# Performance work log

Hardware: AMD Instinct MI355X
Metric: run time of the kernel (lower is better)

The kernel has to match this reference:

```python
import jax, jax.numpy as jnp
import numpy as np

N_NODES = 100000
N_EDGES = 1600000
IN_CH, HID_CH, OUT_CH = 64, 64, 16
N_REL = 8


def setup_inputs() -> dict:
    key = jax.random.key(0)
    ks = jax.random.split(key, 10)
    x = jax.random.normal(ks[0], (N_NODES, IN_CH), dtype=jnp.float32)
    edge_index = jax.random.randint(ks[1], (2, N_EDGES), 0, N_NODES, dtype=jnp.int64)
    edge_type = jax.random.randint(ks[2], (N_EDGES,), 0, N_REL, dtype=jnp.int64)
    # RGCNConv params: per-relation weight, root weight, bias (Glorot-ish scale)
    def glorot(k, shape):
        fan = shape[-2] + shape[-1]
        return jax.random.normal(k, shape, dtype=jnp.float32) * jnp.sqrt(2.0 / fan)
    W1 = glorot(ks[3], (N_REL, IN_CH, HID_CH))
    root1 = glorot(ks[4], (IN_CH, HID_CH))
    b1 = jnp.zeros((HID_CH,), dtype=jnp.float32)
    W2 = glorot(ks[5], (N_REL, HID_CH, OUT_CH))
    root2 = glorot(ks[6], (HID_CH, OUT_CH))
    b2 = jnp.zeros((OUT_CH,), dtype=jnp.float32)
    return {"x": x, "edge_index": edge_index, "edge_type": edge_type,
            "W1": W1, "root1": root1, "b1": b1,
            "W2": W2, "root2": root2, "b2": b2}


def rgcn_conv(x, src, dst, edge_type, W_rel, W_root, bias):
    """PyG RGCNConv: out_i = x_i @ W_root + b + sum_r mean_{j in N_r(i)} x_j @ W_r.
    Mean is linear, so aggregate raw features per relation, then transform."""
    n = x.shape[0]
    xs = x[src]  # [E, F] gathered source features (hot memory-bound op)
    out = x @ W_root + bias
    for r in range(W_rel.shape[0]):  # small fixed relation count
        mask = (edge_type == r).astype(x.dtype)  # [E]
        agg = jax.ops.segment_sum(xs * mask[:, None], dst, num_segments=n)  # [N, F]
        cnt = jax.ops.segment_sum(mask, dst, num_segments=n)  # [N]
        agg = agg / jnp.clip(cnt, 1.0)[:, None]  # mean aggr; 0 when no edges
        out = out + agg @ W_rel[r]
    return out


def reference(x, edge_index, edge_type, W1, root1, b1, W2, root2, b2):
    src, dst = edge_index[0], edge_index[1]
    h = rgcn_conv(x, src, dst, edge_type, W1, root1, b1)
    h = jax.nn.relu(h)
    h = rgcn_conv(h, src, dst, edge_type, W2, root2, b2)
    # global_mean_pool with a single graph: mean over nodes -> [1, out]
    g = jnp.mean(h, axis=0, keepdims=True)
    return jax.nn.log_softmax(g, axis=1)
```

## Files before the change

kernel.cpp:

```cpp
#include <hip/hip_runtime.h>
#include <hip/hip_bf16.h>


#define CH 64
#define BK_EDGES 2048
#define CAP 12288
#define RPT 12

typedef __attribute__((ext_vector_type(8))) short short8;
typedef __attribute__((ext_vector_type(4))) float f32x4;
typedef __attribute__((ext_vector_type(2))) float f32x2;

__device__ inline ushort f2bf(float f) {
    unsigned b = __float_as_uint(f);
    unsigned r = (b + 0x7FFFu + ((b >> 16) & 1u)) >> 16;
    return (ushort)r;
}
__device__ inline float bf2f(ushort u) {
    return __uint_as_float(((unsigned)u) << 16);
}

__device__ inline void acc8fp8(float* a, uint2 w, float m) {
    f32x2 p;
    p = __builtin_amdgcn_cvt_pk_f32_fp8(w.x, 0); a[0] += m * p.x; a[1] += m * p.y;
    p = __builtin_amdgcn_cvt_pk_f32_fp8(w.x, 1); a[2] += m * p.x; a[3] += m * p.y;
    p = __builtin_amdgcn_cvt_pk_f32_fp8(w.y, 0); a[4] += m * p.x; a[5] += m * p.y;
    p = __builtin_amdgcn_cvt_pk_f32_fp8(w.y, 1); a[6] += m * p.x; a[7] += m * p.y;
}


__global__ __launch_bounds__(256) void prep_kernel(
    const int* __restrict__ src, const int* __restrict__ dst,
    const int* __restrict__ etype, const float* __restrict__ x,
    const float* __restrict__ W1, const float* __restrict__ root1,
    int* __restrict__ gBucketCnt, int2* __restrict__ bucket_buf,
    ushort* __restrict__ xbf, unsigned char* __restrict__ xq,
    ushort* __restrict__ wf,
    int E, int N, int nBin, int nXbf)
{
    __shared__ int s_k[BK_EDGES];
    __shared__ int s_y[BK_EDGES];
    __shared__ int hist[256], scanv[256], lcur[256], bstart[256], gbase[256];
    const int t = threadIdx.x;
    const int bid = blockIdx.x;

    if (bid >= nBin) {
        if (bid < nBin + nXbf) {
            int i = (bid - nBin) * 256 + t;
            if (i < N * CH / 4) {
                float4 v = ((const float4*)x)[i];
                ((ushort4*)xbf)[i] = make_ushort4(f2bf(v.x), f2bf(v.y), f2bf(v.z), f2bf(v.w));
                int p8 = __builtin_amdgcn_cvt_pk_fp8_f32(v.x, v.y, 0, 0);
                p8 = __builtin_amdgcn_cvt_pk_fp8_f32(v.z, v.w, p8, 1);
                ((unsigned int*)xq)[i] = (unsigned int)p8;
            }
        } else {
            int idx = (bid - nBin - nXbf) * 256 + t;
            if (idx < 9 * 2 * 4 * 64 * 8) {
                int j    = idx & 7;
                int lane = (idx >> 3) & 63;
                int ct   = (idx >> 9) & 3;
                int ks   = (idx >> 11) & 1;
                int rel  = idx >> 12;
                int k = ks * 32 + (lane >> 4) * 8 + j;
                int n = ct * 16 + (lane & 15);
                float v = (rel < 8) ? W1[((size_t)rel * 64 + k) * 64 + n]
                                    : root1[(size_t)k * 64 + n];
                wf[idx] = f2bf(v);
            }
        }
        return;
    }

    const int e0 = bid * BK_EDGES;
    const int cnt = min(BK_EDGES, E - e0);

    hist[t] = 0;
    __syncthreads();

    int myb[8], myk[8], myy[8];
    #pragma unroll
    for (int i = 0; i < 8; ++i) {
        int li = t + i * 256;
        if (li < cnt) {
            int e = e0 + li;
            int r = etype[e];
            int k = r * N + dst[e];
            myk[i] = k;
            myy[i] = (r << 17) | src[e];
            myb[i] = k >> 12;
            atomicAdd(&hist[myb[i]], 1);
        } else myb[i] = -1;
    }
    __syncthreads();

    int v = hist[t];
    scanv[t] = v;
    __syncthreads();
    for (int off = 1; off < 256; off <<= 1) {
        int u = (t >= off) ? scanv[t - off] : 0;
        __syncthreads();
        scanv[t] += u;
        __syncthreads();
    }
    int excl = scanv[t] - v;
    bstart[t] = excl;
    lcur[t] = excl;
    __syncthreads();

    #pragma unroll
    for (int i = 0; i < 8; ++i) {
        if (myb[i] >= 0) {
            int p = atomicAdd(&lcur[myb[i]], 1);
            s_k[p] = myk[i];
            s_y[p] = myy[i];
        }
    }
    __syncthreads();

    if (v > 0) gbase[t] = atomicAdd(&gBucketCnt[t], v);
    __syncthreads();

    for (int p = t; p < cnt; p += 256) {
        int k = s_k[p];
        int b = k >> 12;
        int gp = gbase[b] + (p - bstart[b]);
        if (gp < CAP)
            bucket_buf[(size_t)b * CAP + gp] = make_int2(k, s_y[p]);
    }
}


__global__ __launch_bounds__(1024) void build_kernel(
    const int2* __restrict__ bucket_buf, const int* __restrict__ gBucketCnt,
    int* __restrict__ rowptr, float* __restrict__ inv,
    int* __restrict__ perm, float* __restrict__ kappa, int N)
{
    __shared__ int hist[4096];
    __shared__ int cur[4096];
    __shared__ int part[1024];
    const int b = blockIdx.x;
    const int t = threadIdx.x;
    const int nb = min(gBucketCnt[b], CAP);
    const int2* rec = bucket_buf + (size_t)b * CAP;

    int rk[RPT], ry[RPT];
    #pragma unroll
    for (int i = 0; i < RPT; ++i) {
        int j = t + i * 1024;
        if (j < nb) { int2 v = rec[j]; rk[i] = v.x; ry[i] = v.y; }
        else        { rk[i] = -1; ry[i] = 0; }
    }

    int bc = (t < 256) ? gBucketCnt[t] : 0;
    part[t] = bc;
    __syncthreads();
    for (int off = 1; off < 1024; off <<= 1) {
        int u = (t >= off) ? part[t - off] : 0;
        __syncthreads();
        part[t] += u;
        __syncthreads();
    }
    __shared__ int baseS;
    if (t == b) baseS = part[t] - bc;
    __syncthreads();
    const int base = baseS;

    for (int i = t; i < 4096; i += 1024) hist[i] = 0;
    __syncthreads();
    #pragma unroll
    for (int i = 0; i < RPT; ++i)
        if (rk[i] >= 0) atomicAdd(&hist[rk[i] & 4095], 1);
    __syncthreads();

    const int i0 = t * 4;
    int h0 = hist[i0], h1 = hist[i0 + 1], h2 = hist[i0 + 2], h3 = hist[i0 + 3];
    int s = h0 + h1 + h2 + h3;
    part[t] = s;
    __syncthreads();
    for (int off = 1; off < 1024; off <<= 1) {
        int u = (t >= off) ? part[t - off] : 0;
        __syncthreads();
        part[t] += u;
        __syncthreads();
    }
    int run = base + part[t] - s;
    int hk[4] = {h0, h1, h2, h3};
    #pragma unroll
    for (int k = 0; k < 4; ++k) {
        cur[i0 + k] = run;
        rowptr[b * 4096 + i0 + k] = run;
        inv[b * 4096 + i0 + k] = 1.0f / (float)max(hk[k], 1);
        run += hk[k];
    }
    __syncthreads();

    #pragma unroll
    for (int i = 0; i < RPT; ++i) {
        if (rk[i] >= 0) {
            int pos = atomicAdd(&cur[rk[i] & 4095], 1);
            perm[pos] = ry[i] & 0x1FFFF;
        }
    }

    #pragma unroll
    for (int i = 0; i < RPT; ++i) {
        if (rk[i] >= 0) {
            float iv = 1.0f / (float)hist[rk[i] & 4095];
            unsafeAtomicAdd(&kappa[((ry[i] & 0x1FFFF) << 3) | (ry[i] >> 17)], iv);
        }
    }
}


__global__ __launch_bounds__(256) void rgcn1_fused_kernel(
    const int* __restrict__ rowptr, const int* __restrict__ perm,
    const float* __restrict__ inv, const ushort* __restrict__ xbf,
    const unsigned char* __restrict__ xq,
    const ushort* __restrict__ wfrag, const float* __restrict__ b1,
    ushort* __restrict__ h, int N)
{
    __shared__ ushort Abuf[4][16 * 72];
    __shared__ int    rpS[4][144];
    __shared__ float  invS[4][128];
    const int widx = threadIdx.x >> 6;
    const int lane = threadIdx.x & 63;
    const int wid = (blockIdx.x << 2) | widx;
    const int base = wid << 4;
    if (base >= N) return;

    const int m0 = lane & 15;
    const int q  = lane >> 4;
    const int sg = lane >> 3;
    const int cg = lane & 7;
    ushort* ab = Abuf[widx];
    int*    rpL = rpS[widx];
    float*  ivL = invS[widx];

    for (int i = lane; i < 136; i += 64) {
        int r = i / 17, mm = i - r * 17;
        rpL[i] = rowptr[(size_t)r * N + base + mm];
    }
    for (int i = lane; i < 128; i += 64)
        ivL[i] = inv[(size_t)(i >> 4) * N + base + (i & 15)];

    f32x4 acc4[4];
    #pragma unroll
    for (int ct = 0; ct < 4; ++ct) acc4[ct] = (f32x4)(0.0f);

    for (int r = 0; r < 8; ++r) {
        const int iA = r * 17 + sg;
        const int iB = iA + 8;
        int jA = rpL[iA], eA = rpL[iA + 1];
        int jB = rpL[iB], eB = rpL[iB + 1];
        float a[8] = {}, bacc[8] = {};
        int s0A = perm[(jA     < eA) ? jA     : 0];
        int s1A = perm[(jA + 1 < eA) ? jA + 1 : 0];
        int s0B = perm[(jB     < eB) ? jB     : 0];
        int s1B = perm[(jB + 1 < eB) ? jB + 1 : 0];
        while (jA < eA || jB < eB) {
            uint2 w0A = *(const uint2*)(xq + (size_t)s0A * CH + (cg << 3));
            uint2 w1A = *(const uint2*)(xq + (size_t)s1A * CH + (cg << 3));
            uint2 w0B = *(const uint2*)(xq + (size_t)s0B * CH + (cg << 3));
            uint2 w1B = *(const uint2*)(xq + (size_t)s1B * CH + (cg << 3));
            int t0A = perm[(jA + 2 < eA) ? jA + 2 : 0];
            int t1A = perm[(jA + 3 < eA) ? jA + 3 : 0];
            int t0B = perm[(jB + 2 < eB) ? jB + 2 : 0];
            int t1B = perm[(jB + 3 < eB) ? jB + 3 : 0];
            float m0A = (jA     < eA) ? 1.f : 0.f;
            float m1A = (jA + 1 < eA) ? 1.f : 0.f;
            float m0B = (jB     < eB) ? 1.f : 0.f;
            float m1B = (jB + 1 < eB) ? 1.f : 0.f;
            acc8fp8(a,    w0A, m0A);
            acc8fp8(a,    w1A, m1A);
            acc8fp8(bacc, w0B, m0B);
            acc8fp8(bacc, w1B, m1B);
            s0A = t0A; s1A = t1A; s0B = t0B; s1B = t1B;
            jA += 2; jB += 2;
        }
        const float ivA = ivL[(r << 4) | sg];
        const float ivB = ivL[(r << 4) | (8 + sg)];
        short8 oA, oB;
        #pragma unroll
        for (int k = 0; k < 8; ++k) {
            oA[k] = (short)f2bf(a[k] * ivA);
            oB[k] = (short)f2bf(bacc[k] * ivB);
        }
        *(short8*)&ab[sg * 72 + (cg << 3)]       = oA;
        *(short8*)&ab[(8 + sg) * 72 + (cg << 3)] = oB;

        #pragma unroll
        for (int s = 0; s < 2; ++s) {
            short8 av = *(short8*)&ab[m0 * 72 + s * 32 + q * 8];
            #pragma unroll
            for (int ct = 0; ct < 4; ++ct) {
                short8 bv = *(const short8*)&wfrag[(((size_t)(r * 2 + s) * 4 + ct) * 64 + lane) * 8];
                acc4[ct] = __builtin_amdgcn_mfma_f32_16x16x32_bf16(av, bv, acc4[ct], 0, 0, 0);
            }
        }
    }

    {
        int node = min(base + m0, N - 1);
        #pragma unroll
        for (int s = 0; s < 2; ++s) {
            short8 av = *(const short8*)&xbf[(size_t)node * CH + s * 32 + q * 8];
            #pragma unroll
            for (int ct = 0; ct < 4; ++ct) {
                short8 bv = *(const short8*)&wfrag[(((size_t)(8 * 2 + s) * 4 + ct) * 64 + lane) * 8];
                acc4[ct] = __builtin_amdgcn_mfma_f32_16x16x32_bf16(av, bv, acc4[ct], 0, 0, 0);
            }
        }
    }

    #pragma unroll
    for (int ct = 0; ct < 4; ++ct) {
        int c = ct * 16 + m0;
        float bb = b1[c];
        #pragma unroll
        for (int v = 0; v < 4; ++v) {
            int node = base + q * 4 + v;
            if (node < N)
                h[(size_t)node * CH + c] = f2bf(fmaxf(acc4[ct][v] + bb, 0.f));
        }
    }
}


__global__ __launch_bounds__(256) void kred_kernel(
    const ushort* __restrict__ h, const float* __restrict__ kappa,
    float* __restrict__ sacc, int N)
{
    const int lane = threadIdx.x & 63;
    const int w = threadIdx.x >> 6;
    int wave = (blockIdx.x << 2) | w;
    const int wstride = gridDim.x << 2;
    float racc[9] = {};
    for (int i = wave; i < N; i += wstride) {
        float hv = bf2f(h[(size_t)i * CH + lane]);
        #pragma unroll
        for (int r = 0; r < 8; ++r) racc[r] += hv * kappa[i * 8 + r];
        racc[8] += hv;
    }
    __shared__ float red[4][9][64];
    #pragma unroll
    for (int r = 0; r < 9; ++r) red[w][r][lane] = racc[r];
    __syncthreads();
    if (w == 0) {
        #pragma unroll
        for (int r = 0; r < 9; ++r) {
            float s4 = red[0][r][lane] + red[1][r][lane] + red[2][r][lane] + red[3][r][lane];
            unsafeAtomicAdd(&sacc[r * 64 + lane], s4);
        }
    }
}

__global__ void finalize_kernel(const float* __restrict__ sacc, const float* __restrict__ root2,
                                const float* __restrict__ W2, const float* __restrict__ b2,
                                float* __restrict__ out, float invN)
{
    __shared__ float g[16];
    int t = threadIdx.x;
    if (t < 16) {
        const float* s0 = sacc + 512;
        float acc = 0.f;
        for (int c = 0; c < 64; ++c) acc += s0[c] * root2[c * 16 + t];
        for (int r = 0; r < 8; ++r) {
            const float* sr = sacc + r * 64;
            for (int c = 0; c < 64; ++c) acc += sr[c] * W2[(r * 64 + c) * 16 + t];
        }
        g[t] = acc * invN + b2[t];
    }
    __syncthreads();
    if (t < 16) {
        float m = -1e30f;
        for (int i = 0; i < 16; ++i) m = fmaxf(m, g[i]);
        float s = 0.f;
        for (int i = 0; i < 16; ++i) s += expf(g[i] - m);
        out[t] = g[t] - (m + logf(s));
    }
}


extern "C" void kernel_launch(void* const* d_in, const int* in_sizes, int n_in,
                              void* d_out, int out_size, void* d_ws, size_t ws_size,
                              hipStream_t stream)
{
    const float* x     = (const float*)d_in[0];
    const int*   eidx  = (const int*)d_in[1];
    const int*   etype = (const int*)d_in[2];
    const float* W1    = (const float*)d_in[3];
    const float* root1 = (const float*)d_in[4];
    const float* b1    = (const float*)d_in[5];
    const float* W2    = (const float*)d_in[6];
    const float* root2 = (const float*)d_in[7];
    const float* b2    = (const float*)d_in[8];
    float* out = (float*)d_out;

    const int E = in_sizes[1] / 2;
    const int N = in_sizes[0] / CH;
    const int NKEY = N * 8;
    const int NBUK = (NKEY + 4095) / 4096;
    const int KSPACE = NBUK << 12;
    const int* srcI = eidx;
    const int* dstI = eidx + E;

    int* wsi = (int*)d_ws;
    int*   gBucketCnt = wsi;
    float* sacc       = (float*)(gBucketCnt + 256);
    float* kappa      = sacc + 576;
    float* inv        = kappa + NKEY;
    int*   rowptr     = (int*)(inv + KSPACE);
    int*   perm       = rowptr + KSPACE + 16;
    size_t off = (size_t)((perm + E) - wsi);
    off = (off + 1) & ~(size_t)1;
    int2*  bucket_buf = (int2*)(wsi + off);
    off += (size_t)NBUK * CAP * 2;
    off = (off + 7) & ~(size_t)7;
    ushort* xbf = (ushort*)(wsi + off);
    ushort* wfg = xbf + (size_t)N * CH;
    unsigned char* xq = (unsigned char*)(wfg + 36864);
    ushort* h = (ushort*)(xq + (size_t)N * CH);

    hipMemsetAsync(d_ws, 0, (size_t)(256 + 576 + NKEY) * 4, stream);

    const int nBin = (E + BK_EDGES - 1) / BK_EDGES;
    const int nXbf = (N * CH / 4 + 255) / 256;
    const int nWf  = (36864 + 255) / 256;
    prep_kernel<<<nBin + nXbf + nWf, 256, 0, stream>>>(
        srcI, dstI, etype, x, W1, root1, gBucketCnt, bucket_buf, xbf, xq, wfg,
        E, N, nBin, nXbf);

    build_kernel<<<NBUK, 1024, 0, stream>>>(
        bucket_buf, gBucketCnt, rowptr, inv, perm, kappa, N);

    const int tiles = (N + 15) / 16;
    rgcn1_fused_kernel<<<(tiles + 3) / 4, 256, 0, stream>>>(
        rowptr, perm, inv, xbf, xq, wfg, b1, h, N);

    kred_kernel<<<1024, 256, 0, stream>>>(h, kappa, sacc, N);
    finalize_kernel<<<1, 64, 0, stream>>>(sacc, root2, W2, b2, out, 1.0f / (float)N);
}
```

Before: 328.6 us.

## Move kappa scatter from build kernel into dedicated blocks of fused layer-1 kernel

The per-edge kappa accumulation (atomic adds of inverse degree per source/relation) is removed from the build kernel and done by 128 extra blocks prepended to the fused layer-1 kernel grid. Those blocks re-read the bucket records and the precomputed inv array instead of the shared-memory histogram. The intent is to shorten the serial build kernel and overlap the atomic scatter with the layer-1 gather/MMA work. The cost is an extra pass over the bucket buffer, and the atomics now compete with the main kernel for bandwidth.

```diff
diff --git a/kernel.cpp b/kernel.cpp
--- a/kernel.cpp
+++ b/kernel.cpp
@@ -6,6 +6,7 @@
 #define BK_EDGES 2048
 #define CAP 12288
 #define RPT 12
+#define KB 128
 
 typedef __attribute__((ext_vector_type(8))) short short8;
 typedef __attribute__((ext_vector_type(4))) float f32x4;
@@ -134,7 +135,7 @@
 __global__ __launch_bounds__(1024) void build_kernel(
     const int2* __restrict__ bucket_buf, const int* __restrict__ gBucketCnt,
     int* __restrict__ rowptr, float* __restrict__ inv,
-    int* __restrict__ perm, float* __restrict__ kappa, int N)
+    int* __restrict__ perm, int N)
 {
     __shared__ int hist[4096];
     __shared__ int cur[4096];
@@ -202,14 +203,6 @@
             perm[pos] = ry[i] & 0x1FFFF;
         }
     }
-
-    #pragma unroll
-    for (int i = 0; i < RPT; ++i) {
-        if (rk[i] >= 0) {
-            float iv = 1.0f / (float)hist[rk[i] & 4095];
-            unsafeAtomicAdd(&kappa[((ry[i] & 0x1FFFF) << 3) | (ry[i] >> 17)], iv);
-        }
-    }
 }
 
 
@@ -218,14 +211,29 @@
     const float* __restrict__ inv, const ushort* __restrict__ xbf,
     const unsigned char* __restrict__ xq,
     const ushort* __restrict__ wfrag, const float* __restrict__ b1,
-    ushort* __restrict__ h, int N)
-{
+    const int2* __restrict__ bucket_buf, const int* __restrict__ gBucketCnt,
+    float* __restrict__ kappa,
+    ushort* __restrict__ h, int N, int nbuk)
+{
+    if (blockIdx.x < KB) {
+        for (int b = blockIdx.x; b < nbuk; b += KB) {
+            const int nb = min(gBucketCnt[b], CAP);
+            const int2* rec = bucket_buf + (size_t)b * CAP;
+            for (int j = (int)threadIdx.x; j < nb; j += 256) {
+                int2 v = rec[j];
+                float iv = inv[v.x];
+                unsafeAtomicAdd(&kappa[((v.y & 0x1FFFF) << 3) | (v.y >> 17)], iv);
+            }
+        }
+        return;
+    }
+
     __shared__ ushort Abuf[4][16 * 72];
     __shared__ int    rpS[4][144];
     __shared__ float  invS[4][128];
     const int widx = threadIdx.x >> 6;
     const int lane = threadIdx.x & 63;
-    const int wid = (blockIdx.x << 2) | widx;
+    const int wid = ((blockIdx.x - KB) << 2) | widx;
     const int base = wid << 4;
     if (base >= N) return;
 
@@ -432,11 +440,12 @@
         E, N, nBin, nXbf);
 
     build_kernel<<<NBUK, 1024, 0, stream>>>(
-        bucket_buf, gBucketCnt, rowptr, inv, perm, kappa, N);
+        bucket_buf, gBucketCnt, rowptr, inv, perm, N);
 
     const int tiles = (N + 15) / 16;
-    rgcn1_fused_kernel<<<(tiles + 3) / 4, 256, 0, stream>>>(
-        rowptr, perm, inv, xbf, xq, wfg, b1, h, N);
+    rgcn1_fused_kernel<<<KB + (tiles + 3) / 4, 256, 0, stream>>>(
+        rowptr, perm, inv, xbf, xq, wfg, b1, bucket_buf, gBucketCnt, kappa,
+        h, N, NBUK);
 
     kred_kernel<<<1024, 256, 0, stream>>>(h, kappa, sacc, N);
     finalize_kernel<<<1, 64, 0, stream>>>(sacc, root2, W2, b2, out, 1.0f / (float)N);
```

New measurement: 280.7 us. -14.6%, faster.
